# Optimization experiments

Hardware: AMD Instinct MI355X
Metric: run time of the kernel (lower is better)

The kernel has to match this reference:

```python
import jax, jax.numpy as jnp
import numpy as np

B, NIN, H, W, DIN = 4, 32, 14, 14, 8
NOUT, DOUT, K, STRIDE = 32, 16, 3, 1
PROJ = NOUT * DOUT  # 512


def setup_inputs() -> dict:
    key = jax.random.key(0)
    ks = jax.random.split(key, 4)
    return {
        "x": jax.random.normal(ks[0], (B, NIN, H, W, DIN), jnp.float32),
        "W1": jax.random.normal(ks[1], (DIN, PROJ), jnp.float32) * 0.1,
        "b1": jnp.zeros((PROJ,), jnp.float32),
        "W2": jax.random.normal(ks[2], (PROJ, 128), jnp.float32) * 0.05,
        "b2": jnp.zeros((128,), jnp.float32),
        "W3": jax.random.normal(ks[3], (128, PROJ), jnp.float32) * 0.1,
        "b3": jnp.zeros((PROJ,), jnp.float32),
    }


def _squash(x, axis=-1):
    ns = jnp.sum(x * x, axis=axis, keepdims=True)
    return (ns / (1.0 + ns)) * x / jnp.sqrt(ns + 1e-16)


def reference(x, W1, b1, W2, b2, W3, b3):
    oH = (H - K) // STRIDE + 1
    oW = (W - K) // STRIDE + 1
    # patch extraction: (B,NIN,oH,oW,K,K,DIN)
    idx = (jnp.arange(oH) * STRIDE)[:, None] + jnp.arange(K)[None, :]
    p = x[:, :, idx]                 # (B,NIN,oH,K,W,DIN)
    p = p[:, :, :, :, idx]           # (B,NIN,oH,K,oW,K,DIN)
    p = jnp.transpose(p, (0, 1, 2, 4, 3, 5, 6))
    # projector MLP (applied to last dim)
    h = jax.nn.relu(p @ W1 + b1)
    h = jax.nn.relu(h @ W2 + b2)
    preds = h @ W3 + b3              # (B,NIN,oH,oW,K,K,PROJ)
    preds = preds.reshape(B, NIN, oH, oW, K, K, NOUT, DOUT)
    preds = jnp.transpose(preds, (0, 1, 4, 5, 6, 2, 3, 7))
    preds = preds.reshape(B, NIN * K * K, NOUT, oH, oW, DOUT)
    # dynamic routing (3 iterations)
    b_ij = jnp.zeros((B, NIN * K * K, NOUT, oH, oW, 1), preds.dtype)
    c_ij = None
    v_j = None
    for i in range(3):
        c_ij = jax.nn.softmax(b_ij, axis=2)
        s_j = jnp.sum(c_ij * preds, axis=1, keepdims=True)
        v_j = _squash(s_j, axis=-1)
        if i < 2:
            b_ij = b_ij + jnp.sum(preds * v_j, axis=-1, keepdims=True)
    # c_ij: squeeze(5).unsqueeze(3) -> (B,Nc,NOUT,1,oH,oW), then entropy over NOUT
    c = jnp.squeeze(c_ij, 5)[:, :, :, None]
    ent = -jnp.sum(c * jnp.log(c + 1e-16), axis=2) / jnp.log(float(NOUT))
    return jnp.squeeze(v_j, 1), ent
```

## Files before the change

### kernel.cpp

```cpp
#include <hip/hip_runtime.h>
#include <hip/hip_bf16.h>

#define B_ 4
#define NIN_ 32
#define H_ 14
#define W_ 14
#define DIN_ 8
#define NOUT_ 32
#define DOUT_ 16
#define K_ 3
#define OH_ 12
#define OW_ 12
#define PROJ_ 512
#define HID_ 128
#define M_ 288
#define NPIX_ (B_*NIN_*H_*W_)

typedef __attribute__((ext_vector_type(8))) short short8;
typedef __attribute__((ext_vector_type(4))) float f32x4;

__device__ __forceinline__ float bflo(unsigned int u) { return __uint_as_float(u << 16); }
__device__ __forceinline__ float bfhi(unsigned int u) { return __uint_as_float(u & 0xffff0000u); }
__device__ __forceinline__ float bf2f(unsigned short u) { return __uint_as_float(((unsigned int)u) << 16); }
__device__ __forceinline__ unsigned short bfbits(float f) {
    __hip_bfloat16 h = __float2bfloat16(f);
    return *(unsigned short*)&h;
}

__global__ __launch_bounds__(256) void prep_kernel(
    const float* __restrict__ W2, const float* __restrict__ W3,
    __hip_bfloat16* __restrict__ W2B, __hip_bfloat16* __restrict__ W3B)
{
    int idx = blockIdx.x * 256 + threadIdx.x;
    {
        int j = idx & 7, lane = (idx >> 3) & 63, kt = (idx >> 9) & 15, nt = idx >> 13;
        int k = kt * 32 + (lane >> 4) * 8 + j;
        int c = nt * 16 + (lane & 15);
        W2B[idx] = __float2bfloat16(W2[k * HID_ + c]);
    }
    {
        int j = idx & 7, lane = (idx >> 3) & 63, kt = (idx >> 9) & 3, nt = idx >> 11;
        int k = kt * 32 + (lane >> 4) * 8 + j;
        int c = nt * 16 + (lane & 15);
        W3B[idx] = __float2bfloat16(W3[k * PROJ_ + c]);
    }
}

__global__ __launch_bounds__(256) void mlp_mfma_kernel(
    const float* __restrict__ x,
    const float* __restrict__ W1, const float* __restrict__ b1,
    const short8* __restrict__ W2B, const float* __restrict__ b2,
    const short8* __restrict__ W3B, const float* __restrict__ b3,
    __hip_bfloat16* __restrict__ U)
{
    __shared__ short smem[33792];
    short* h1A = smem;
    float (*xin)[8] = (float(*)[8])(smem + 32768);

    const int t = threadIdx.x;
    const int pix0 = blockIdx.x * 64;
    const int l = t & 63, wv = t >> 6;

    {
        int idx = t;
        #pragma unroll
        for (int rep = 0; rep < 2; ++rep, idx += 256) {
            int p = idx >> 3, c = idx & 7;
            xin[p][c] = x[(pix0 + p) * DIN_ + c];
        }
    }

    {
        const int k0 = 2 * t;
        float w0[8], w1[8];
        #pragma unroll
        for (int c = 0; c < 8; ++c) {
            w0[c] = W1[c * PROJ_ + k0];
            w1[c] = W1[c * PROJ_ + k0 + 1];
        }
        const float bb0 = b1[k0], bb1 = b1[k0 + 1];
        const int kt = k0 >> 5, hi = (k0 >> 3) & 3, j = k0 & 7;
        const int base_k = (kt * 64 + hi * 16) * 8 + j;
        unsigned int* h1w = (unsigned int*)h1A;
        __syncthreads();
        for (int p = 0; p < 64; ++p) {
            float4 xa = *(const float4*)&xin[p][0];
            float4 xb = *(const float4*)&xin[p][4];
            float a0 = bb0 + xa.x*w0[0] + xa.y*w0[1] + xa.z*w0[2] + xa.w*w0[3]
                           + xb.x*w0[4] + xb.y*w0[5] + xb.z*w0[6] + xb.w*w0[7];
            float a1 = bb1 + xa.x*w1[0] + xa.y*w1[1] + xa.z*w1[2] + xa.w*w1[3]
                           + xb.x*w1[4] + xb.y*w1[5] + xb.z*w1[6] + xb.w*w1[7];
            a0 = fmaxf(a0, 0.f); a1 = fmaxf(a1, 0.f);
            unsigned int packed = (unsigned int)bfbits(a0)
                                | ((unsigned int)bfbits(a1) << 16);
            int flat = (p >> 4) * 8192 + base_k + (p & 15) * 8;
            h1w[flat >> 1] = packed;
        }
    }
    __syncthreads();

    f32x4 acc2[8];
    {
        const short8* h1f = (const short8*)h1A;
        #pragma unroll
        for (int nt = 0; nt < 8; ++nt) acc2[nt] = (f32x4){0.f, 0.f, 0.f, 0.f};
        for (int ktk = 0; ktk < 16; ++ktk) {
            short8 a = h1f[(wv * 16 + ktk) * 64 + l];
            #pragma unroll
            for (int nt = 0; nt < 8; ++nt) {
                short8 b = W2B[(nt * 16 + ktk) * 64 + l];
                acc2[nt] = __builtin_amdgcn_mfma_f32_16x16x32_bf16(a, b, acc2[nt], 0, 0, 0);
            }
        }
    }
    __syncthreads();
    short* h2A = smem;
    {
        const int r0 = (l >> 4) * 4;
        #pragma unroll
        for (int nt = 0; nt < 8; ++nt) {
            int c = nt * 16 + (l & 15);
            float bb = b2[c];
            int kt3 = c >> 5;
            int lane3base = ((c >> 3) & 3) * 16;
            #pragma unroll
            for (int q = 0; q < 4; ++q) {
                float v = fmaxf(acc2[nt][q] + bb, 0.f);
                int flat = ((wv * 4 + kt3) * 64 + lane3base + r0 + q) * 8 + (c & 7);
                h2A[flat] = (short)bfbits(v);
            }
        }
    }
    __syncthreads();

    {
        const short8* h2f = (const short8*)h2A;
        short8 a[4];
        #pragma unroll
        for (int ktk = 0; ktk < 4; ++ktk) a[ktk] = h2f[(wv * 4 + ktk) * 64 + l];
        const int r0 = (l >> 4) * 4;
        for (int pass = 0; pass < 4; ++pass) {
            f32x4 acc[8];
            #pragma unroll
            for (int nt2 = 0; nt2 < 8; ++nt2) acc[nt2] = (f32x4){0.f, 0.f, 0.f, 0.f};
            #pragma unroll
            for (int nt2 = 0; nt2 < 8; ++nt2) {
                int nt = pass * 8 + nt2;
                #pragma unroll
                for (int ktk = 0; ktk < 4; ++ktk) {
                    short8 b = W3B[(nt * 4 + ktk) * 64 + l];
                    acc[nt2] = __builtin_amdgcn_mfma_f32_16x16x32_bf16(a[ktk], b, acc[nt2], 0, 0, 0);
                }
            }
            #pragma unroll
            for (int nt2 = 0; nt2 < 8; ++nt2) {
                int c = (pass * 8 + nt2) * 16 + (l & 15);
                float bb = b3[c];
                #pragma unroll
                for (int q = 0; q < 4; ++q) {
                    U[(size_t)(pix0 + wv * 16 + r0 + q) * PROJ_ + c] =
                        __float2bfloat16(acc[nt2][q] + bb);
                }
            }
        }
    }
}

__global__ __launch_bounds__(256) void sumn_kernel(
    const unsigned int* __restrict__ U32, unsigned int* __restrict__ SumNb)
{
    const int byx = blockIdx.x;
    const int b = byx / 196, yx = byx % 196;
    const int t = threadIdx.x;
    const unsigned int* p = U32 + ((size_t)(b * NIN_) * 196 + yx) * 256 + t;
    float a0 = 0.f, a1 = 0.f;
    #pragma unroll 8
    for (int n = 0; n < NIN_; ++n) {
        unsigned int u = p[(size_t)n * 196 * 256];
        a0 += bflo(u); a1 += bfhi(u);
    }
    SumNb[(size_t)byx * 256 + t] =
        (unsigned int)bfbits(a0) | ((unsigned int)bfbits(a1) << 16);
}

__global__ __launch_bounds__(512) void route_kernel(
    const __hip_bfloat16* __restrict__ Ub,
    const unsigned short* __restrict__ SumNb,
    float* __restrict__ out_v,
    float* __restrict__ out_ent)
{
    const uint4* __restrict__ U4 = (const uint4*)Ub;

    __shared__ int   pixoff[M_];
    __shared__ float sredT[16][16][33];
    __shared__ float sbufT[16][33];
    __shared__ float vvT[16][33];
    __shared__ float scl[NOUT_];

    const int bid = blockIdx.x;
    const int xcd = bid & 7, sub = bid >> 3;
    const int b  = xcd >> 1;
    const int ij = (xcd & 1) * 72 + sub;
    const int i  = ij / OW_, j = ij % OW_;
    const int t  = threadIdx.x;
    const int l  = t & 63, wv = t >> 6;
    const int no = l & 31, half = l >> 5;
    const int hw = wv * 2 + half;

    if (t < M_) {
        int n = t / 9, r = t % 9, ki = r / 3, kj = r % 3;
        pixoff[t] = ((b * NIN_ + n) * H_ + (i + ki)) * W_ + (j + kj);
    }
    {
        float s = 0.f;
        const int base = b * 196;
        #pragma unroll
        for (int ki = 0; ki < 3; ++ki)
            #pragma unroll
            for (int kj = 0; kj < 3; ++kj)
                s += bf2f(SumNb[(size_t)(base + (i + ki) * 14 + (j + kj)) * 512 + t]);
        sbufT[t & 15][t >> 4] = s * (1.f / 32.f);
    }
    __syncthreads();
    if (t < NOUT_) {
        float ns = 0.f;
        #pragma unroll
        for (int d = 0; d < DOUT_; ++d) { float s = sbufT[d][t]; ns += s * s; }
        scl[t] = ns / (1.f + ns) * rsqrtf(ns + 1e-16f);
    }
    __syncthreads();
    vvT[t >> 5][t & 31] = sbufT[t >> 5][t & 31] * scl[t & 31];
    __syncthreads();

    float vr[16];
    #pragma unroll
    for (int k = 0; k < 16; ++k) vr[k] = vvT[k][no];

    const int mbase = wv * 36;

    for (int pass = 1; pass <= 2; ++pass) {
        float s_acc[16];
        #pragma unroll
        for (int k = 0; k < 16; ++k) s_acc[k] = 0.f;

        uint4 p0, p1;
        {
            size_t base = (size_t)pixoff[mbase + half] * 64 + no * 2;
            p0 = U4[base]; p1 = U4[base + 1];
        }
        for (int c = 0; c < 18; ++c) {
            uint4 q0 = p0, q1 = p1;
            if (c + 1 < 18) {
                size_t base = (size_t)pixoff[mbase + 2 * (c + 1) + half] * 64 + no * 2;
                p0 = U4[base]; p1 = U4[base + 1];
            }
            float pv[16];
            pv[0]=bflo(q0.x);  pv[1]=bfhi(q0.x);  pv[2]=bflo(q0.y);  pv[3]=bfhi(q0.y);
            pv[4]=bflo(q0.z);  pv[5]=bfhi(q0.z);  pv[6]=bflo(q0.w);  pv[7]=bfhi(q0.w);
            pv[8]=bflo(q1.x);  pv[9]=bfhi(q1.x);  pv[10]=bflo(q1.y); pv[11]=bfhi(q1.y);
            pv[12]=bflo(q1.z); pv[13]=bfhi(q1.z); pv[14]=bflo(q1.w); pv[15]=bfhi(q1.w);

            float d0 = pv[0]*vr[0] + pv[4]*vr[4] + pv[8]*vr[8]  + pv[12]*vr[12];
            float d1 = pv[1]*vr[1] + pv[5]*vr[5] + pv[9]*vr[9]  + pv[13]*vr[13];
            float d2 = pv[2]*vr[2] + pv[6]*vr[6] + pv[10]*vr[10]+ pv[14]*vr[14];
            float d3 = pv[3]*vr[3] + pv[7]*vr[7] + pv[11]*vr[11]+ pv[15]*vr[15];
            float dp = (d0 + d1) + (d2 + d3);

            float e = __expf(dp);
            float S = e;
            if (pass == 2) {
                float E = e * dp;
                #pragma unroll
                for (int msk = 16; msk >= 1; msk >>= 1) {
                    S += __shfl_xor(S, msk);
                    E += __shfl_xor(E, msk);
                }
                if (no == 0)
                    out_ent[(b * M_ + (mbase + 2 * c + half)) * (OH_ * OW_) + ij] =
                        (__logf(S) - E / S) * 0.28853900817779268f;
                float cc = e * __frcp_rn(S);
                #pragma unroll
                for (int k = 0; k < 16; ++k) s_acc[k] += cc * pv[k];
            } else {
                #pragma unroll
                for (int msk = 16; msk >= 1; msk >>= 1)
                    S += __shfl_xor(S, msk);
                float cc = e * __frcp_rn(S);
                #pragma unroll
                for (int k = 0; k < 16; ++k) s_acc[k] += cc * pv[k];
            }
        }

        #pragma unroll
        for (int k = 0; k < 16; ++k) sredT[hw][k][no] = s_acc[k];
        __syncthreads();
        {
            int d = t >> 5, n2 = t & 31;
            float ssm = 0.f;
            #pragma unroll
            for (int h2 = 0; h2 < 16; ++h2) ssm += sredT[h2][d][n2];
            sbufT[d][n2] = ssm;
        }
        __syncthreads();
        if (t < NOUT_) {
            float ns = 0.f;
            #pragma unroll
            for (int d = 0; d < DOUT_; ++d) { float s = sbufT[d][t]; ns += s * s; }
            scl[t] = ns / (1.f + ns) * rsqrtf(ns + 1e-16f);
        }
        __syncthreads();
        vvT[t >> 5][t & 31] = sbufT[t >> 5][t & 31] * scl[t & 31];
        __syncthreads();

        if (pass == 1) {
            #pragma unroll
            for (int k = 0; k < 16; ++k) vr[k] += vvT[k][no];
        }
    }

    {
        int no2 = t >> 4, d = t & 15;
        out_v[(((b * NOUT_ + no2) * OH_ + i) * OW_ + j) * DOUT_ + d] = vvT[d][no2];
    }
}

extern "C" void kernel_launch(void* const* d_in, const int* in_sizes, int n_in,
                              void* d_out, int out_size, void* d_ws, size_t ws_size,
                              hipStream_t stream) {
    const float* x  = (const float*)d_in[0];
    const float* W1 = (const float*)d_in[1];
    const float* b1 = (const float*)d_in[2];
    const float* W2 = (const float*)d_in[3];
    const float* b2 = (const float*)d_in[4];
    const float* W3 = (const float*)d_in[5];
    const float* b3 = (const float*)d_in[6];

    char* ws = (char*)d_ws;
    __hip_bfloat16* U   = (__hip_bfloat16*)ws;
    __hip_bfloat16* W2B = (__hip_bfloat16*)(ws + (size_t)NPIX_ * PROJ_ * 2);
    __hip_bfloat16* W3B = W2B + (size_t)PROJ_ * HID_;
    unsigned int*   SumNb = (unsigned int*)(W3B + (size_t)PROJ_ * HID_);

    float* out_v   = (float*)d_out;
    float* out_ent = out_v + (size_t)B_ * NOUT_ * OH_ * OW_ * DOUT_;

    hipLaunchKernelGGL(prep_kernel, dim3(256), dim3(256), 0, stream,
                       W2, W3, W2B, W3B);
    hipLaunchKernelGGL(mlp_mfma_kernel, dim3(NPIX_ / 64), dim3(256), 0, stream,
                       x, W1, b1, (const short8*)W2B, b2, (const short8*)W3B, b3, U);
    hipLaunchKernelGGL(sumn_kernel, dim3(B_ * H_ * W_), dim3(256), 0, stream,
                       (const unsigned int*)U, SumNb);
    hipLaunchKernelGGL(route_kernel, dim3(B_ * OH_ * OW_), dim3(512), 0, stream,
                       U, (const unsigned short*)SumNb, out_v, out_ent);
}
```

Before: 103.3 us.

## Move first MLP layer onto MFMA and double-buffer routing loads

The first projector layer (DIN=8 to 512) moves from scalar FMAs onto a bf16 MFMA. The 8-wide input is zero-padded to K=32, and W1 is pre-converted into a bf16 fragment layout in the prep kernel. In the routing kernel, prefetch now runs two iterations ahead with the loop fully unrolled, and the per-wave halves are combined with a cross-lane shuffle before the shared-memory reduction, which halves that reduction buffer. The cost is wasted MFMA work on the padding, bf16 rounding of x and W1, and higher register pressure from the unrolled prefetch.

```diff
diff --git a/kernel.cpp b/kernel.cpp
--- a/kernel.cpp
+++ b/kernel.cpp
@@ -28,8 +28,10 @@
 }
 
 __global__ __launch_bounds__(256) void prep_kernel(
-    const float* __restrict__ W2, const float* __restrict__ W3,
-    __hip_bfloat16* __restrict__ W2B, __hip_bfloat16* __restrict__ W3B)
+    const float* __restrict__ W1, const float* __restrict__ W2,
+    const float* __restrict__ W3,
+    __hip_bfloat16* __restrict__ W1B, __hip_bfloat16* __restrict__ W2B,
+    __hip_bfloat16* __restrict__ W3B)
 {
     int idx = blockIdx.x * 256 + threadIdx.x;
     {
@@ -44,57 +46,63 @@
         int c = nt * 16 + (lane & 15);
         W3B[idx] = __float2bfloat16(W3[k * PROJ_ + c]);
     }
+    if (idx < 16384) {
+        int j = idx & 7, lane = (idx >> 3) & 63, nt = idx >> 9;
+        int c = nt * 16 + (lane & 15);
+        W1B[idx] = (lane < 16) ? __float2bfloat16(W1[j * PROJ_ + c])
+                               : __float2bfloat16(0.f);
+    }
 }
 
 __global__ __launch_bounds__(256) void mlp_mfma_kernel(
     const float* __restrict__ x,
-    const float* __restrict__ W1, const float* __restrict__ b1,
+    const short8* __restrict__ W1B, const float* __restrict__ b1,
     const short8* __restrict__ W2B, const float* __restrict__ b2,
     const short8* __restrict__ W3B, const float* __restrict__ b3,
     __hip_bfloat16* __restrict__ U)
 {
-    __shared__ short smem[33792];
+    __shared__ short smem[34816];
     short* h1A = smem;
-    float (*xin)[8] = (float(*)[8])(smem + 32768);
+    short* A16 = smem + 32768;
 
     const int t = threadIdx.x;
     const int pix0 = blockIdx.x * 64;
     const int l = t & 63, wv = t >> 6;
-
-    {
-        int idx = t;
-        #pragma unroll
-        for (int rep = 0; rep < 2; ++rep, idx += 256) {
-            int p = idx >> 3, c = idx & 7;
-            xin[p][c] = x[(pix0 + p) * DIN_ + c];
-        }
-    }
-
-    {
-        const int k0 = 2 * t;
-        float w0[8], w1[8];
-        #pragma unroll
-        for (int c = 0; c < 8; ++c) {
-            w0[c] = W1[c * PROJ_ + k0];
-            w1[c] = W1[c * PROJ_ + k0 + 1];
-        }
-        const float bb0 = b1[k0], bb1 = b1[k0 + 1];
-        const int kt = k0 >> 5, hi = (k0 >> 3) & 3, j = k0 & 7;
-        const int base_k = (kt * 64 + hi * 16) * 8 + j;
-        unsigned int* h1w = (unsigned int*)h1A;
-        __syncthreads();
-        for (int p = 0; p < 64; ++p) {
-            float4 xa = *(const float4*)&xin[p][0];
-            float4 xb = *(const float4*)&xin[p][4];
-            float a0 = bb0 + xa.x*w0[0] + xa.y*w0[1] + xa.z*w0[2] + xa.w*w0[3]
-                           + xb.x*w0[4] + xb.y*w0[5] + xb.z*w0[6] + xb.w*w0[7];
-            float a1 = bb1 + xa.x*w1[0] + xa.y*w1[1] + xa.z*w1[2] + xa.w*w1[3]
-                           + xb.x*w1[4] + xb.y*w1[5] + xb.z*w1[6] + xb.w*w1[7];
-            a0 = fmaxf(a0, 0.f); a1 = fmaxf(a1, 0.f);
-            unsigned int packed = (unsigned int)bfbits(a0)
-                                | ((unsigned int)bfbits(a1) << 16);
-            int flat = (p >> 4) * 8192 + base_k + (p & 15) * 8;
-            h1w[flat >> 1] = packed;
+    const int r0 = (l >> 4) * 4;
+
+    {
+        int mt = t >> 6, ln = t & 63;
+        unsigned int* d32 = (unsigned int*)(A16 + (mt * 64 + ln) * 8);
+        if (ln < 16) {
+            const float* xr = &x[(size_t)(pix0 + mt * 16 + ln) * DIN_];
+            float4 xa = *(const float4*)xr;
+            float4 xb = *(const float4*)(xr + 4);
+            d32[0] = (unsigned int)bfbits(xa.x) | ((unsigned int)bfbits(xa.y) << 16);
+            d32[1] = (unsigned int)bfbits(xa.z) | ((unsigned int)bfbits(xa.w) << 16);
+            d32[2] = (unsigned int)bfbits(xb.x) | ((unsigned int)bfbits(xb.y) << 16);
+            d32[3] = (unsigned int)bfbits(xb.z) | ((unsigned int)bfbits(xb.w) << 16);
+        } else {
+            d32[0] = 0u; d32[1] = 0u; d32[2] = 0u; d32[3] = 0u;
+        }
+    }
+    __syncthreads();
+
+    {
+        const short8* A16f = (const short8*)A16;
+        short8 a1 = A16f[wv * 64 + l];
+        #pragma unroll
+        for (int nt = 0; nt < 32; ++nt) {
+            f32x4 acc = (f32x4){0.f, 0.f, 0.f, 0.f};
+            acc = __builtin_amdgcn_mfma_f32_16x16x32_bf16(a1, W1B[nt * 64 + l], acc, 0, 0, 0);
+            int c = nt * 16 + (l & 15);
+            float bb = b1[c];
+            int kt = c >> 5, hi = (c >> 3) & 3;
+            #pragma unroll
+            for (int q = 0; q < 4; ++q) {
+                float v = fmaxf(acc[q] + bb, 0.f);
+                int flat = ((wv * 16 + kt) * 64 + hi * 16 + r0 + q) * 8 + (c & 7);
+                h1A[flat] = (short)bfbits(v);
+            }
         }
     }
     __syncthreads();
@@ -116,7 +124,6 @@
     __syncthreads();
     short* h2A = smem;
     {
-        const int r0 = (l >> 4) * 4;
         #pragma unroll
         for (int nt = 0; nt < 8; ++nt) {
             int c = nt * 16 + (l & 15);
@@ -138,7 +145,6 @@
         short8 a[4];
         #pragma unroll
         for (int ktk = 0; ktk < 4; ++ktk) a[ktk] = h2f[(wv * 4 + ktk) * 64 + l];
-        const int r0 = (l >> 4) * 4;
         for (int pass = 0; pass < 4; ++pass) {
             f32x4 acc[8];
             #pragma unroll
@@ -192,7 +198,7 @@
     const uint4* __restrict__ U4 = (const uint4*)Ub;
 
     __shared__ int   pixoff[M_];
-    __shared__ float sredT[16][16][33];
+    __shared__ float sredT[8][16][33];
     __shared__ float sbufT[16][33];
     __shared__ float vvT[16][33];
     __shared__ float scl[NOUT_];
@@ -205,7 +211,6 @@
     const int t  = threadIdx.x;
     const int l  = t & 63, wv = t >> 6;
     const int no = l & 31, half = l >> 5;
-    const int hw = wv * 2 + half;
 
     if (t < M_) {
         int n = t / 9, r = t % 9, ki = r / 3, kj = r % 3;
@@ -243,16 +248,28 @@
         #pragma unroll
         for (int k = 0; k < 16; ++k) s_acc[k] = 0.f;
 
-        uint4 p0, p1;
+        uint4 pa0, pa1, pb0, pb1;
         {
-            size_t base = (size_t)pixoff[mbase + half] * 64 + no * 2;
-            p0 = U4[base]; p1 = U4[base + 1];
-        }
+            size_t ba = (size_t)pixoff[mbase + half] * 64 + no * 2;
+            pa0 = U4[ba]; pa1 = U4[ba + 1];
+            size_t bb2 = (size_t)pixoff[mbase + 2 + half] * 64 + no * 2;
+            pb0 = U4[bb2]; pb1 = U4[bb2 + 1];
+        }
+        #pragma unroll
         for (int c = 0; c < 18; ++c) {
-            uint4 q0 = p0, q1 = p1;
-            if (c + 1 < 18) {
-                size_t base = (size_t)pixoff[mbase + 2 * (c + 1) + half] * 64 + no * 2;
-                p0 = U4[base]; p1 = U4[base + 1];
+            uint4 q0, q1;
+            if ((c & 1) == 0) {
+                q0 = pa0; q1 = pa1;
+                if (c + 2 < 18) {
+                    size_t nb = (size_t)pixoff[mbase + 2 * (c + 2) + half] * 64 + no * 2;
+                    pa0 = U4[nb]; pa1 = U4[nb + 1];
+                }
+            } else {
+                q0 = pb0; q1 = pb1;
+                if (c + 2 < 18) {
+                    size_t nb = (size_t)pixoff[mbase + 2 * (c + 2) + half] * 64 + no * 2;
+                    pb0 = U4[nb]; pb1 = U4[nb + 1];
+                }
             }
             float pv[16];
             pv[0]=bflo(q0.x);  pv[1]=bfhi(q0.x);  pv[2]=bflo(q0.y);  pv[3]=bfhi(q0.y);
@@ -292,13 +309,17 @@
         }
 
         #pragma unroll
-        for (int k = 0; k < 16; ++k) sredT[hw][k][no] = s_acc[k];
+        for (int k = 0; k < 16; ++k) s_acc[k] += __shfl_xor(s_acc[k], 32);
+        if (half == 0) {
+            #pragma unroll
+            for (int k = 0; k < 16; ++k) sredT[wv][k][no] = s_acc[k];
+        }
         __syncthreads();
         {
             int d = t >> 5, n2 = t & 31;
             float ssm = 0.f;
             #pragma unroll
-            for (int h2 = 0; h2 < 16; ++h2) ssm += sredT[h2][d][n2];
+            for (int h2 = 0; h2 < 8; ++h2) ssm += sredT[h2][d][n2];
             sbufT[d][n2] = ssm;
         }
         __syncthreads();
@@ -339,15 +360,17 @@
     __hip_bfloat16* U   = (__hip_bfloat16*)ws;
     __hip_bfloat16* W2B = (__hip_bfloat16*)(ws + (size_t)NPIX_ * PROJ_ * 2);
     __hip_bfloat16* W3B = W2B + (size_t)PROJ_ * HID_;
-    unsigned int*   SumNb = (unsigned int*)(W3B + (size_t)PROJ_ * HID_);
+    __hip_bfloat16* W1B = W3B + (size_t)PROJ_ * HID_;
+    unsigned int*   SumNb = (unsigned int*)(W1B + 16384);
 
     float* out_v   = (float*)d_out;
     float* out_ent = out_v + (size_t)B_ * NOUT_ * OH_ * OW_ * DOUT_;
 
     hipLaunchKernelGGL(prep_kernel, dim3(256), dim3(256), 0, stream,
-                       W2, W3, W2B, W3B);
+                       W1, W2, W3, W1B, W2B, W3B);
     hipLaunchKernelGGL(mlp_mfma_kernel, dim3(NPIX_ / 64), dim3(256), 0, stream,
-                       x, W1, b1, (const short8*)W2B, b2, (const short8*)W3B, b3, U);
+                       x, (const short8*)W1B, b1, (const short8*)W2B, b2,
+                       (const short8*)W3B, b3, U);
     hipLaunchKernelGGL(sumn_kernel, dim3(B_ * H_ * W_), dim3(256), 0, stream,
                        (const unsigned int*)U, SumNb);
     hipLaunchKernelGGL(route_kernel, dim3(B_ * OH_ * OW_), dim3(512), 0, stream,
```

Result: slower. 293.9 us (+184.5%).
